# Performance work log

Measured on AMD Instinct MI355X. Metric: run time of the kernel, lower is better.

Reference implementation:

```python
import jax, jax.numpy as jnp
import numpy as np

SOS = 1
V, H, B, T = 32000, 1024, 32, 64


def setup_inputs() -> dict:
    key = jax.random.key(0)
    ks = jax.random.split(key, 9)
    scale = 1.0 / np.sqrt(H)
    return {
        "encoder_outputs": jax.random.normal(ks[0], (B, T, H), dtype=jnp.float32),
        "encoder_hidden": jax.random.normal(ks[1], (1, B, H), dtype=jnp.float32),
        "target_tensor": jax.random.randint(ks[2], (B, T), 0, V),
        "embedding": jax.random.normal(ks[3], (V, H), dtype=jnp.float32),
        "w_ih": jax.random.uniform(ks[4], (3 * H, H), jnp.float32, -scale, scale),
        "w_hh": jax.random.uniform(ks[5], (3 * H, H), jnp.float32, -scale, scale),
        "b_ih": jax.random.uniform(ks[6], (3 * H,), jnp.float32, -scale, scale),
        "b_hh": jax.random.uniform(ks[7], (3 * H,), jnp.float32, -scale, scale),
        "w_out": jax.random.uniform(ks[8], (V, H), jnp.float32, -scale, scale),
        "b_out": jnp.zeros((V,), dtype=jnp.float32),
    }


def _gru_cell(x, h, w_ih, w_hh, b_ih, b_hh):
    # PyTorch GRU cell: gates ordered (r, z, n)
    gi = x @ w_ih.T + b_ih            # [B, 3H]
    gh = h @ w_hh.T + b_hh            # [B, 3H]
    i_r, i_z, i_n = jnp.split(gi, 3, axis=-1)
    h_r, h_z, h_n = jnp.split(gh, 3, axis=-1)
    r = jax.nn.sigmoid(i_r + h_r)
    z = jax.nn.sigmoid(i_z + h_z)
    n = jnp.tanh(i_n + r * h_n)
    return (1.0 - z) * n + z * h


def reference(encoder_outputs, encoder_hidden, target_tensor, embedding,
              w_ih, w_hh, b_ih, b_hh, w_out, b_out):
    batch = encoder_outputs.shape[0]
    # teacher-forced input tokens: [SOS, y_0, ..., y_{T-2}] -> [T, B]
    sos = jnp.full((batch, 1), SOS, dtype=target_tensor.dtype)
    tokens = jnp.concatenate([sos, target_tensor[:, :-1]], axis=1).T  # [T, B]

    h0 = encoder_hidden[0]  # [B, H]

    def step(h, tok):
        x = jax.nn.relu(embedding[tok])            # [B, H]
        h_new = _gru_cell(x, h, w_ih, w_hh, b_ih, b_hh)
        return h_new, h_new

    h_last, hs = jax.lax.scan(step, h0, tokens)    # hs: [T, B, H]
    logits = jnp.einsum('tbh,vh->btv', hs, w_out) + b_out  # [B, T, V]
    log_probs = jax.nn.log_softmax(logits, axis=-1)
    return log_probs, h_last[None]  # hidden returned as [1, B, H]
```

## Files before the change

kernel.cpp:

```cpp
#include <hip/hip_runtime.h>
#include <stdint.h>

#define Hd 1024
#define Bd 32
#define Td 64
#define Vd 32000
#define TB (Td*Bd)
#define G3H 3072
#define NB 64
#define NPOOL 192
#define JC 16
#define NTILE 250
static const size_t BTV = (size_t)Bd * Td * Vd;

typedef unsigned short u16;
typedef __attribute__((ext_vector_type(8))) short bf16x8;
typedef __attribute__((ext_vector_type(4))) float f32x4;
typedef __attribute__((ext_vector_type(4))) unsigned int u32x4;

typedef __attribute__((address_space(3))) void lds_void;
typedef __attribute__((address_space(1))) const void gbl_void;

__device__ __forceinline__ void async_ld16(const void* g, void* l) {
    __builtin_amdgcn_global_load_lds((gbl_void*)g, (lds_void*)l, 16, 0, 0);
}

__device__ __forceinline__ u16 f2bf(float f) {
    union { float f; uint32_t u; } v; v.f = f;
    uint32_t u = v.u;
    return (u16)((u + 0x7fffu + ((u >> 16) & 1u)) >> 16);
}

__device__ __forceinline__ u32x4 gload_b128_sc(const u16* p) {
    u32x4 r;
    asm volatile("global_load_dwordx4 %0, %1, off sc0 sc1"
                 : "=v"(r) : "v"(p) : "memory");
    return r;
}
__device__ __forceinline__ void gstore_b32_sc(u16* p, unsigned int v) {
    asm volatile("global_store_dword %0, %1, off sc0 sc1"
                 :: "v"(p), "v"(v) : "memory");
}
__device__ __forceinline__ void gstore_u32_sc(unsigned int* p, unsigned int v) {
    asm volatile("global_store_dword %0, %1, off sc0 sc1"
                 :: "v"(p), "v"(v) : "memory");
}

__device__ __forceinline__ float fsigmoid(float x) {
    return __builtin_amdgcn_rcpf(1.f + __expf(-x));
}
__device__ __forceinline__ float ftanh(float x) {
    return 1.f - 2.f * __builtin_amdgcn_rcpf(1.f + __expf(2.f * x));
}

__global__ void k_conv_bf16(const float* __restrict__ src, u16* __restrict__ dst, int n4) {
    int i = blockIdx.x * blockDim.x + threadIdx.x;
    if (i >= n4) return;
    float4 f = ((const float4*)src)[i];
    ushort4 o;
    o.x = f2bf(f.x); o.y = f2bf(f.y); o.z = f2bf(f.z); o.w = f2bf(f.w);
    ((ushort4*)dst)[i] = o;
}

__global__ void k_embed(const float* __restrict__ emb, const int* __restrict__ tgt,
                        u16* __restrict__ Xb) {
    int r = blockIdx.x;
    int t = r >> 5, b = r & 31;
    int tok = (t == 0) ? 1 : tgt[b * Td + (t - 1)];
    const float4* srow = (const float4*)(emb + (size_t)tok * Hd);
    int k = threadIdx.x;
    float4 f = srow[k];
    ushort4 o;
    o.x = f2bf(fmaxf(f.x, 0.f)); o.y = f2bf(fmaxf(f.y, 0.f));
    o.z = f2bf(fmaxf(f.z, 0.f)); o.w = f2bf(fmaxf(f.w, 0.f));
    ((ushort4*)(Xb + (size_t)r * Hd))[k] = o;
}

__global__ void k_init_h(const float* __restrict__ eh, u16* __restrict__ hb,
                         unsigned int* __restrict__ cnt) {
    if (blockIdx.x == 0 && threadIdx.x < NB) cnt[threadIdx.x] = 0u;
    int i = blockIdx.x * blockDim.x + threadIdx.x;
    float4 f = ((const float4*)eh)[i];
    ushort4 o;
    o.x = f2bf(f.x); o.y = f2bf(f.y); o.z = f2bf(f.z); o.w = f2bf(f.w);
    ((ushort4*)hb)[i] = o;
}

template<int MODE, int SWAP>
__global__ __launch_bounds__(256, 2)
void k_gemm128(const u16* __restrict__ A, const u16* __restrict__ Bm,
               const float* __restrict__ bias, float* __restrict__ C,
               int N, int K)
{
    __shared__ alignas(16) u16 As[128 * 32];
    __shared__ alignas(16) u16 Bs[128 * 32];
    const int tid  = threadIdx.x;
    const int wave = tid >> 6;
    const int lane = tid & 63;
    const int l16  = lane & 15;
    const int q    = lane >> 4;
    const int wm   = (wave & 1) << 6;
    const int wn   = (wave >> 1) << 6;
    const int tm   = (SWAP ? blockIdx.x : blockIdx.y) << 7;
    const int tn   = (SWAP ? blockIdx.y : blockIdx.x) << 7;

    f32x4 acc[4][4];
#pragma unroll
    for (int i = 0; i < 4; ++i)
#pragma unroll
        for (int j = 0; j < 4; ++j) { f32x4 z = {0.f,0.f,0.f,0.f}; acc[i][j] = z; }

    const int c0 = wave * 2, c1 = wave * 2 + 1;
    const int cr = lane >> 2;
    const int kg = lane & 3;
    const u16* gA0 = A + (size_t)(tm + c0*16 + cr) * K + kg*8;
    const u16* gA1 = A + (size_t)(tm + c1*16 + cr) * K + kg*8;
    const u16* gB0 = Bm + (size_t)(tn + c0*16 + cr) * K + kg*8;
    const u16* gB1 = Bm + (size_t)(tn + c1*16 + cr) * K + kg*8;
    u16* lA0 = &As[c0*512 + lane*8];
    u16* lA1 = &As[c1*512 + lane*8];
    u16* lB0 = &Bs[c0*512 + lane*8];
    u16* lB1 = &Bs[c1*512 + lane*8];

    for (int k0 = 0; k0 < K; k0 += 32) {
        async_ld16(gA0 + k0, lA0);
        async_ld16(gA1 + k0, lA1);
        async_ld16(gB0 + k0, lB0);
        async_ld16(gB1 + k0, lB1);
        __syncthreads();
        bf16x8 af[4], bfr[4];
#pragma unroll
        for (int i = 0; i < 4; ++i)
            af[i] = *(const bf16x8*)&As[(wm + i*16 + l16) * 32 + q*8];
#pragma unroll
        for (int j = 0; j < 4; ++j)
            bfr[j] = *(const bf16x8*)&Bs[(wn + j*16 + l16) * 32 + q*8];
#pragma unroll
        for (int i = 0; i < 4; ++i)
#pragma unroll
            for (int j = 0; j < 4; ++j)
                acc[i][j] = __builtin_amdgcn_mfma_f32_16x16x32_bf16(af[i], bfr[j], acc[i][j], 0, 0, 0);
        __syncthreads();
    }

#pragma unroll
    for (int i = 0; i < 4; ++i) {
        const int mbase = tm + wm + i*16 + q*4;
#pragma unroll
        for (int j = 0; j < 4; ++j) {
            const int n = tn + wn + j*16 + l16;
            const float bv = bias[n];
#pragma unroll
            for (int r = 0; r < 4; ++r) {
                const int m = mbase + r;
                const float v = acc[i][j][r] + bv;
                if (MODE == 0) {
                    C[(size_t)m * N + n] = v;
                } else {
                    const int tt = m >> 5, bb = m & 31;
                    C[(size_t)((bb << 6) + tt) * Vd + n] = v;
                }
            }
        }
    }
}

__global__ __launch_bounds__(256, 1)
void k_gru_logits(const float* __restrict__ gi,
                  const float* __restrict__ enc_h,
                  const u16* __restrict__ w_hhb,
                  const float* __restrict__ b_hh,
                  u16* __restrict__ hbA, u16* __restrict__ hbB,
                  u16* __restrict__ hsb, float* __restrict__ hlast,
                  unsigned int* __restrict__ cnt,
                  const u16* __restrict__ w_outb,
                  const float* __restrict__ b_out,
                  float* __restrict__ out)
{
    __shared__ alignas(16) unsigned char SM[111360];
    const int tid  = threadIdx.x;
    const int wave = tid >> 6, lane = tid & 63;
    const int l16  = lane & 15, q = lane >> 4;

    if (blockIdx.x < NB) {
        u16* Ws = (u16*)SM;
        typedef float ghs_t[3][32][17];
        ghs_t* ghs = (ghs_t*)(SM + 98304);
        const int j0 = blockIdx.x * JC;

        for (int idx = tid; idx < 48 * 128; idx += 256) {
            int gr = idx >> 7;
            int c  = idx & 127;
            const u16* src = w_hhb + (size_t)((gr >> 4) * Hd + j0 + (gr & 15)) * Hd + c * 8;
            *(bf16x8*)&Ws[(size_t)(c * 48 + gr) * 8] = *(const bf16x8*)src;
        }

        const int b  = tid >> 3;
        const int jp = (tid & 7) * 2;
        float h0 = enc_h[b * Hd + j0 + jp];
        float h1 = enc_h[b * Hd + j0 + jp + 1];
        const float br0 = b_hh[j0 + jp],           br1 = b_hh[j0 + jp + 1];
        const float bz0 = b_hh[Hd + j0 + jp],      bz1 = b_hh[Hd + j0 + jp + 1];
        const float bn0 = b_hh[2*Hd + j0 + jp],    bn1 = b_hh[2*Hd + j0 + jp + 1];

        const int mh = wave & 1, kh = wave >> 1;

        float gr0, gr1, gz0, gz1, gn0, gn1;
        {
            const float* gir = gi + (size_t)b * G3H;
            gr0 = gir[j0 + jp];        gr1 = gir[j0 + jp + 1];
            gz0 = gir[Hd + j0 + jp];   gz1 = gir[Hd + j0 + jp + 1];
            gn0 = gir[2*Hd + j0 + jp]; gn1 = gir[2*Hd + j0 + jp + 1];
        }

        __syncthreads();

        for (int t = 0; t < Td; ++t) {
            const u16* hb_in  = (t & 1) ? hbB : hbA;
            u16*       hb_out = (t & 1) ? hbA : hbB;
            const int row = t * 32 + b;

            const u16* ap = hb_in + (size_t)(mh*16 + l16) * Hd + kh*512 + q*8;
            u32x4 areg[16];
#pragma unroll
            for (int it = 0; it < 16; ++it)
                areg[it] = gload_b128_sc(ap + it*32);

            asm volatile("s_waitcnt vmcnt(0)" ::: "memory");

            f32x4 acc0 = {0.f,0.f,0.f,0.f}, acc1 = acc0, acc2 = acc0;
#pragma unroll
            for (int it = 0; it < 16; ++it) {
                bf16x8 a = __builtin_bit_cast(bf16x8, areg[it]);
                const int kgrp = kh*64 + it*4 + q;
                const u16* wp = &Ws[(size_t)(kgrp * 48 + l16) * 8];
                bf16x8 w0 = *(const bf16x8*)(wp);
                bf16x8 w1 = *(const bf16x8*)(wp + 16*8);
                bf16x8 w2 = *(const bf16x8*)(wp + 32*8);
                acc0 = __builtin_amdgcn_mfma_f32_16x16x32_bf16(a, w0, acc0, 0, 0, 0);
                acc1 = __builtin_amdgcn_mfma_f32_16x16x32_bf16(a, w1, acc1, 0, 0, 0);
                acc2 = __builtin_amdgcn_mfma_f32_16x16x32_bf16(a, w2, acc2, 0, 0, 0);
            }
#pragma unroll
            for (int r = 0; r < 4; ++r) {
                const int bb = mh*16 + q*4 + r;
                ghs[kh][0][bb][l16] = acc0[r];
                ghs[kh][1][bb][l16] = acc1[r];
                ghs[kh][2][bb][l16] = acc2[r];
            }
            __syncthreads();

            {
                const float hr0 = ghs[0][0][b][jp]   + ghs[1][0][b][jp]   + br0;
                const float hr1 = ghs[0][0][b][jp+1] + ghs[1][0][b][jp+1] + br1;
                const float hz0 = ghs[0][1][b][jp]   + ghs[1][1][b][jp]   + bz0;
                const float hz1 = ghs[0][1][b][jp+1] + ghs[1][1][b][jp+1] + bz1;
                const float hn0 = ghs[0][2][b][jp]   + ghs[1][2][b][jp]   + bn0;
                const float hn1 = ghs[0][2][b][jp+1] + ghs[1][2][b][jp+1] + bn1;
                const float rg0 = fsigmoid(gr0 + hr0);
                const float rg1 = fsigmoid(gr1 + hr1);
                const float zg0 = fsigmoid(gz0 + hz0);
                const float zg1 = fsigmoid(gz1 + hz1);
                const float ng0 = ftanh(gn0 + rg0 * hn0);
                const float ng1 = ftanh(gn1 + rg1 * hn1);
                h0 = (1.f - zg0) * ng0 + zg0 * h0;
                h1 = (1.f - zg1) * ng1 + zg1 * h1;
                ushort2 pv; pv.x = f2bf(h0); pv.y = f2bf(h1);
                const unsigned int pw = (unsigned int)pv.x | ((unsigned int)pv.y << 16);
                gstore_b32_sc(&hb_out[b * Hd + j0 + jp], pw);
                gstore_b32_sc(&hsb[(size_t)row * Hd + j0 + jp], pw);
                if (t == Td - 1) {
                    hlast[b * Hd + j0 + jp]     = h0;
                    hlast[b * Hd + j0 + jp + 1] = h1;
                }
            }

            __syncthreads();
            if (tid == 0)
                gstore_u32_sc(&cnt[blockIdx.x], (unsigned)(t + 1));

            if (t < Td - 1) {
                {
                    const float* gir = gi + (size_t)((t + 1) * 32 + b) * G3H;
                    gr0 = gir[j0 + jp];        gr1 = gir[j0 + jp + 1];
                    gz0 = gir[Hd + j0 + jp];   gz1 = gir[Hd + j0 + jp + 1];
                    gn0 = gir[2*Hd + j0 + jp]; gn1 = gir[2*Hd + j0 + jp + 1];
                }
                if (wave == 0) {
                    const unsigned tgt = (unsigned)(t + 1);
                    while (!__all(__hip_atomic_load(&cnt[lane], __ATOMIC_RELAXED,
                                                    __HIP_MEMORY_SCOPE_AGENT) >= tgt))
                        __builtin_amdgcn_s_sleep(2);
                }
                __syncthreads();
            }
        }
        return;
    }

    {
        u16* As = (u16*)SM;
        u16* Bs = (u16*)(SM + 32768);
        const int g     = blockIdx.x - NB;
        const int tile0 = g;
        const int tile1 = g + NPOOL;
        const bool two  = (tile1 < NTILE);

        const int wm = (wave & 1) << 6;
        const int wn = (wave >> 1) << 6;
        const int c0 = wave * 2, c1 = wave * 2 + 1;
        const int cr = lane >> 2;
        const int kg = lane & 3;
        const u16* gB0a = w_outb + (size_t)(tile0*128 + c0*16 + cr) * Hd + kg*8;
        const u16* gB1a = w_outb + (size_t)(tile0*128 + c1*16 + cr) * Hd + kg*8;
        const u16* gB0b = w_outb + (size_t)((two ? tile1 : tile0)*128 + c0*16 + cr) * Hd + kg*8;
        const u16* gB1b = w_outb + (size_t)((two ? tile1 : tile0)*128 + c1*16 + cr) * Hd + kg*8;

        const int arow  = tid >> 1;
        const int ahalf = tid & 1;

        for (int G = 0; G < 16; ++G) {
            if (wave == 0) {
                const unsigned tgt = (unsigned)(4 * (G + 1));
                while (!__all(__hip_atomic_load(&cnt[lane], __ATOMIC_RELAXED,
                                                __HIP_MEMORY_SCOPE_AGENT) >= tgt))
                    __builtin_amdgcn_s_sleep(8);
            }
            __syncthreads();

            f32x4 acc0[4][4], acc1[4][4];
#pragma unroll
            for (int i = 0; i < 4; ++i)
#pragma unroll
                for (int j = 0; j < 4; ++j) {
                    f32x4 z = {0.f,0.f,0.f,0.f};
                    acc0[i][j] = z; acc1[i][j] = z;
                }

            const size_t arow0 = (size_t)G * 128;

            for (int s = 0; s < 8; ++s) {
                const int k0 = s * 128;
                const u16* asrc = hsb + (arow0 + arow) * Hd + k0 + ahalf * 64;
                u32x4 ar[8];
#pragma unroll
                for (int j = 0; j < 8; ++j)
                    ar[j] = gload_b128_sc(asrc + j*8);
#pragma unroll
                for (int kc = 0; kc < 4; ++kc) {
                    const int kk = k0 + kc*32;
                    u16* base0 = &Bs[(0*4 + kc) * 4096];
                    async_ld16(gB0a + kk, base0 + c0*512 + lane*8);
                    async_ld16(gB1a + kk, base0 + c1*512 + lane*8);
                    if (two) {
                        u16* base1 = &Bs[(1*4 + kc) * 4096];
                        async_ld16(gB0b + kk, base1 + c0*512 + lane*8);
                        async_ld16(gB1b + kk, base1 + c1*512 + lane*8);
                    }
                }
                asm volatile("s_waitcnt vmcnt(0)" ::: "memory");
#pragma unroll
                for (int j = 0; j < 8; ++j) {
                    const int ob = (ahalf*128 + j*16) ^ ((arow & 7) << 4);
                    *(u32x4*)((unsigned char*)As + arow*256 + ob) = ar[j];
                }
                __syncthreads();

#pragma unroll
                for (int kc = 0; kc < 4; ++kc) {
                    bf16x8 af[4];
#pragma unroll
                    for (int i = 0; i < 4; ++i) {
                        const int row = wm + i*16 + l16;
                        const int ob  = (kc*64 + q*16) ^ ((row & 7) << 4);
                        af[i] = *(const bf16x8*)((const unsigned char*)As + row*256 + ob);
                    }
                    bf16x8 b0[4];
#pragma unroll
                    for (int j = 0; j < 4; ++j)
                        b0[j] = *(const bf16x8*)&Bs[(0*4 + kc)*4096 + (wn + j*16 + l16)*32 + q*8];
#pragma unroll
                    for (int i = 0; i < 4; ++i)
#pragma unroll
                        for (int j = 0; j < 4; ++j)
                            acc0[i][j] = __builtin_amdgcn_mfma_f32_16x16x32_bf16(af[i], b0[j], acc0[i][j], 0, 0, 0);
                    if (two) {
                        bf16x8 b1[4];
#pragma unroll
                        for (int j = 0; j < 4; ++j)
                            b1[j] = *(const bf16x8*)&Bs[(1*4 + kc)*4096 + (wn + j*16 + l16)*32 + q*8];
#pragma unroll
                        for (int i = 0; i < 4; ++i)
#pragma unroll
                            for (int j = 0; j < 4; ++j)
                                acc1[i][j] = __builtin_amdgcn_mfma_f32_16x16x32_bf16(af[i], b1[j], acc1[i][j], 0, 0, 0);
                    }
                }
                __syncthreads();
            }

#pragma unroll
            for (int i = 0; i < 4; ++i) {
                const int lmbase = wm + i*16 + q*4;
#pragma unroll
                for (int j = 0; j < 4; ++j) {
                    const int n0 = tile0*128 + wn + j*16 + l16;
                    const float bv0 = b_out[n0];
#pragma unroll
                    for (int r = 0; r < 4; ++r) {
                        const int gr = (int)(G*128) + lmbase + r;
                        const int tt = gr >> 5, bb = gr & 31;
                        out[(size_t)((bb << 6) + tt) * Vd + n0] = acc0[i][j][r] + bv0;
                    }
                }
            }
            if (two) {
#pragma unroll
                for (int i = 0; i < 4; ++i) {
                    const int lmbase = wm + i*16 + q*4;
#pragma unroll
                    for (int j = 0; j < 4; ++j) {
                        const int n1 = tile1*128 + wn + j*16 + l16;
                        const float bv1 = b_out[n1];
#pragma unroll
                        for (int r = 0; r < 4; ++r) {
                            const int gr = (int)(G*128) + lmbase + r;
                            const int tt = gr >> 5, bb = gr & 31;
                            out[(size_t)((bb << 6) + tt) * Vd + n1] = acc1[i][j][r] + bv1;
                        }
                    }
                }
            }
        }
    }
}

__global__ __launch_bounds__(256)
void k_logsoftmax(float* __restrict__ out) {
    float* row = out + (size_t)blockIdx.x * Vd;
    const int tid = threadIdx.x;
    float m = -1e30f, s = 0.f;
    for (int i = tid * 4; i + 3 < Vd; i += 1024) {
        float4 f = *(const float4*)(row + i);
        float lm = fmaxf(fmaxf(f.x, f.y), fmaxf(f.z, f.w));
        if (lm > m) { s *= __expf(m - lm); m = lm; }
        s += __expf(f.x - m) + __expf(f.y - m) + __expf(f.z - m) + __expf(f.w - m);
    }
    for (int off = 32; off > 0; off >>= 1) {
        float mo = __shfl_down(m, off, 64);
        float so = __shfl_down(s, off, 64);
        float M = fmaxf(m, mo);
        s = s * __expf(m - M) + so * __expf(mo - M);
        m = M;
    }
    __shared__ float sm[4], ss[4];
    const int wave = tid >> 6, lane = tid & 63;
    if (lane == 0) { sm[wave] = m; ss[wave] = s; }
    __syncthreads();
    const float M = fmaxf(fmaxf(sm[0], sm[1]), fmaxf(sm[2], sm[3]));
    const float S = ss[0]*__expf(sm[0]-M) + ss[1]*__expf(sm[1]-M)
                  + ss[2]*__expf(sm[2]-M) + ss[3]*__expf(sm[3]-M);
    const float lz = M + logf(S);
    for (int i = tid * 4; i + 3 < Vd; i += 1024) {
        float4 f = *(const float4*)(row + i);
        f.x -= lz; f.y -= lz; f.z -= lz; f.w -= lz;
        *(float4*)(row + i) = f;
    }
}

extern "C" void kernel_launch(void* const* d_in, const int* in_sizes, int n_in,
                              void* d_out, int out_size, void* d_ws, size_t ws_size,
                              hipStream_t stream) {
    const float* enc_h = (const float*)d_in[1];
    const int*   tgt   = (const int*)d_in[2];
    const float* emb   = (const float*)d_in[3];
    const float* w_ih  = (const float*)d_in[4];
    const float* w_hh  = (const float*)d_in[5];
    const float* b_ih  = (const float*)d_in[6];
    const float* b_hh  = (const float*)d_in[7];
    const float* w_out = (const float*)d_in[8];
    const float* b_out = (const float*)d_in[9];
    float* out = (float*)d_out;

    char* ws = (char*)d_ws;
    size_t off = 0;
    auto alloc = [&](size_t bytes) { void* p = ws + off; off += (bytes + 255) & ~(size_t)255; return p; };
    u16*   w_outb = (u16*)  alloc((size_t)Vd * Hd * 2);
    u16*   w_ihb  = (u16*)  alloc((size_t)G3H * Hd * 2);
    u16*   w_hhb  = (u16*)  alloc((size_t)G3H * Hd * 2);
    u16*   Xb     = (u16*)  alloc((size_t)TB * Hd * 2);
    u16*   hsb    = (u16*)  alloc((size_t)TB * Hd * 2);
    float* gi     = (float*)alloc((size_t)TB * G3H * 4);
    u16*   hb0    = (u16*)  alloc((size_t)Bd * Hd * 2);
    u16*   hb1    = (u16*)  alloc((size_t)Bd * Hd * 2);
    unsigned int* cnt = (unsigned int*) alloc(256);
    (void)ws_size; (void)in_sizes; (void)n_in; (void)out_size;

    k_conv_bf16<<<(Vd*Hd/4 + 255)/256, 256, 0, stream>>>(w_out, w_outb, Vd*Hd/4);
    k_conv_bf16<<<(G3H*Hd/4 + 255)/256, 256, 0, stream>>>(w_ih, w_ihb, G3H*Hd/4);
    k_conv_bf16<<<(G3H*Hd/4 + 255)/256, 256, 0, stream>>>(w_hh, w_hhb, G3H*Hd/4);
    k_embed<<<TB, 256, 0, stream>>>(emb, tgt, Xb);
    k_init_h<<<32, 256, 0, stream>>>(enc_h, hb0, cnt);

    k_gemm128<0,0><<<dim3(G3H/128, TB/128), 256, 0, stream>>>(Xb, w_ihb, b_ih, gi, G3H, Hd);

    k_gru_logits<<<NB + NPOOL, 256, 0, stream>>>(gi, enc_h, w_hhb, b_hh, hb0, hb1,
                                                 hsb, out + BTV, cnt,
                                                 w_outb, b_out, out);

    k_logsoftmax<<<TB, 256, 0, stream>>>(out);
}
```

Before: 1.186 ms.

## Use atomic work queue with double-buffered 256x128 logits tiles in GRU pool

The logits pool blocks now take work items (a 256-row group by 128-column tile) from a global atomic counter, replacing the fixed two-tile assignment per block. Each wave keeps its A fragments in registers and loads them straight from global memory. B tiles are double-buffered in LDS with an XOR swizzle, so the next k-slice can load while MFMAs run. The aim is better load balance across the 250 tiles and overlap of memory with compute. The cost is coarser dependency granularity, since each item waits for 8 GRU steps instead of 4, plus one atomic and two barriers per item.

```diff
diff --git a/kernel.cpp b/kernel.cpp
--- a/kernel.cpp
+++ b/kernel.cpp
@@ -11,6 +11,7 @@
 #define NPOOL 192
 #define JC 16
 #define NTILE 250
+#define NITEMS 2000
 static const size_t BTV = (size_t)Bd * Td * Vd;
 
 typedef unsigned short u16;
@@ -78,7 +79,7 @@
 
 __global__ void k_init_h(const float* __restrict__ eh, u16* __restrict__ hb,
                          unsigned int* __restrict__ cnt) {
-    if (blockIdx.x == 0 && threadIdx.x < NB) cnt[threadIdx.x] = 0u;
+    if (blockIdx.x == 0 && threadIdx.x < 128) cnt[threadIdx.x] = 0u;
     int i = blockIdx.x * blockDim.x + threadIdx.x;
     float4 f = ((const float4*)eh)[i];
     ushort4 o;
@@ -299,135 +300,105 @@
     }
 
     {
-        u16* As = (u16*)SM;
-        u16* Bs = (u16*)(SM + 32768);
-        const int g     = blockIdx.x - NB;
-        const int tile0 = g;
-        const int tile1 = g + NPOOL;
-        const bool two  = (tile1 < NTILE);
-
-        const int wm = (wave & 1) << 6;
-        const int wn = (wave >> 1) << 6;
-        const int c0 = wave * 2, c1 = wave * 2 + 1;
+        u16* Bs = (u16*)SM;
+        volatile unsigned* qw = (volatile unsigned*)(SM + 65536);
         const int cr = lane >> 2;
         const int kg = lane & 3;
-        const u16* gB0a = w_outb + (size_t)(tile0*128 + c0*16 + cr) * Hd + kg*8;
-        const u16* gB1a = w_outb + (size_t)(tile0*128 + c1*16 + cr) * Hd + kg*8;
-        const u16* gB0b = w_outb + (size_t)((two ? tile1 : tile0)*128 + c0*16 + cr) * Hd + kg*8;
-        const u16* gB1b = w_outb + (size_t)((two ? tile1 : tile0)*128 + c1*16 + cr) * Hd + kg*8;
-
-        const int arow  = tid >> 1;
-        const int ahalf = tid & 1;
-
-        for (int G = 0; G < 16; ++G) {
+        const int c0 = wave * 2, c1 = wave * 2 + 1;
+        const int kgs = (kg ^ (cr & 3)) * 8;
+
+        for (;;) {
+            if (tid == 0) *qw = atomicAdd(&cnt[64], 1u);
+            __syncthreads();
+            const unsigned w = *qw;
+            __syncthreads();
+            if (w >= (unsigned)NITEMS) break;
+            const int G8   = (int)(w / (unsigned)NTILE);
+            const int tile = (int)(w % (unsigned)NTILE);
+
             if (wave == 0) {
-                const unsigned tgt = (unsigned)(4 * (G + 1));
+                const unsigned tgt = (unsigned)(8 * (G8 + 1));
                 while (!__all(__hip_atomic_load(&cnt[lane], __ATOMIC_RELAXED,
                                                 __HIP_MEMORY_SCOPE_AGENT) >= tgt))
                     __builtin_amdgcn_s_sleep(8);
             }
             __syncthreads();
 
-            f32x4 acc0[4][4], acc1[4][4];
+            const int rowbase = G8 * 256 + wave * 64;
+            const u16* Ab  = hsb + (size_t)(rowbase + l16) * Hd + q * 8;
+            const u16* Bg0 = w_outb + (size_t)(tile*128 + c0*16 + cr) * Hd + kgs;
+            const u16* Bg1 = w_outb + (size_t)(tile*128 + c1*16 + cr) * Hd + kgs;
+            u16* Bd0 = Bs + (c0*16 + cr)*32 + kg*8;
+            u16* Bd1 = Bs + (c1*16 + cr)*32 + kg*8;
+
+            f32x4 acc[4][8];
 #pragma unroll
             for (int i = 0; i < 4; ++i)
 #pragma unroll
-                for (int j = 0; j < 4; ++j) {
-                    f32x4 z = {0.f,0.f,0.f,0.f};
-                    acc0[i][j] = z; acc1[i][j] = z;
-                }
-
-            const size_t arow0 = (size_t)G * 128;
-
+                for (int j = 0; j < 8; ++j) { f32x4 z = {0.f,0.f,0.f,0.f}; acc[i][j] = z; }
+
+            u32x4 areg[2][4][4];
+#pragma unroll
+            for (int kc = 0; kc < 4; ++kc) {
+                async_ld16(Bg0 + kc*32, Bd0 + kc*4096);
+                async_ld16(Bg1 + kc*32, Bd1 + kc*4096);
+            }
+#pragma unroll
+            for (int i = 0; i < 4; ++i)
+#pragma unroll
+                for (int kc = 0; kc < 4; ++kc)
+                    areg[0][i][kc] = gload_b128_sc(Ab + (size_t)i*16*Hd + kc*32);
+
+#pragma unroll
             for (int s = 0; s < 8; ++s) {
-                const int k0 = s * 128;
-                const u16* asrc = hsb + (arow0 + arow) * Hd + k0 + ahalf * 64;
-                u32x4 ar[8];
-#pragma unroll
-                for (int j = 0; j < 8; ++j)
-                    ar[j] = gload_b128_sc(asrc + j*8);
+                const int cur = s & 1, nxt = cur ^ 1;
+                if (s < 7) {
+                    const int k0 = (s + 1) * 128;
+#pragma unroll
+                    for (int kc = 0; kc < 4; ++kc) {
+                        async_ld16(Bg0 + k0 + kc*32, Bd0 + nxt*16384 + kc*4096);
+                        async_ld16(Bg1 + k0 + kc*32, Bd1 + nxt*16384 + kc*4096);
+                    }
+#pragma unroll
+                    for (int i = 0; i < 4; ++i)
+#pragma unroll
+                        for (int kc = 0; kc < 4; ++kc)
+                            areg[nxt][i][kc] = gload_b128_sc(Ab + (size_t)i*16*Hd + k0 + kc*32);
+                    asm volatile("s_waitcnt vmcnt(24)" ::: "memory");
+                } else {
+                    asm volatile("s_waitcnt vmcnt(0)" ::: "memory");
+                }
+                __builtin_amdgcn_sched_barrier(0);
+                __builtin_amdgcn_s_barrier();
 #pragma unroll
                 for (int kc = 0; kc < 4; ++kc) {
-                    const int kk = k0 + kc*32;
-                    u16* base0 = &Bs[(0*4 + kc) * 4096];
-                    async_ld16(gB0a + kk, base0 + c0*512 + lane*8);
-                    async_ld16(gB1a + kk, base0 + c1*512 + lane*8);
-                    if (two) {
-                        u16* base1 = &Bs[(1*4 + kc) * 4096];
-                        async_ld16(gB0b + kk, base1 + c0*512 + lane*8);
-                        async_ld16(gB1b + kk, base1 + c1*512 + lane*8);
+#pragma unroll
+                    for (int j = 0; j < 8; ++j) {
+                        const int n = j*16 + l16;
+                        const bf16x8 bj = *(const bf16x8*)
+                            &Bs[cur*16384 + kc*4096 + n*32 + (q ^ (n & 3))*8];
+#pragma unroll
+                        for (int i = 0; i < 4; ++i)
+                            acc[i][j] = __builtin_amdgcn_mfma_f32_16x16x32_bf16(
+                                __builtin_bit_cast(bf16x8, areg[cur][i][kc]), bj,
+                                acc[i][j], 0, 0, 0);
                     }
                 }
-                asm volatile("s_waitcnt vmcnt(0)" ::: "memory");
-#pragma unroll
-                for (int j = 0; j < 8; ++j) {
-                    const int ob = (ahalf*128 + j*16) ^ ((arow & 7) << 4);
-                    *(u32x4*)((unsigned char*)As + arow*256 + ob) = ar[j];
-                }
-                __syncthreads();
-
-#pragma unroll
-                for (int kc = 0; kc < 4; ++kc) {
-                    bf16x8 af[4];
-#pragma unroll
-                    for (int i = 0; i < 4; ++i) {
-                        const int row = wm + i*16 + l16;
-                        const int ob  = (kc*64 + q*16) ^ ((row & 7) << 4);
-                        af[i] = *(const bf16x8*)((const unsigned char*)As + row*256 + ob);
-                    }
-                    bf16x8 b0[4];
-#pragma unroll
-                    for (int j = 0; j < 4; ++j)
-                        b0[j] = *(const bf16x8*)&Bs[(0*4 + kc)*4096 + (wn + j*16 + l16)*32 + q*8];
-#pragma unroll
-                    for (int i = 0; i < 4; ++i)
-#pragma unroll
-                        for (int j = 0; j < 4; ++j)
-                            acc0[i][j] = __builtin_amdgcn_mfma_f32_16x16x32_bf16(af[i], b0[j], acc0[i][j], 0, 0, 0);
-                    if (two) {
-                        bf16x8 b1[4];
-#pragma unroll
-                        for (int j = 0; j < 4; ++j)
-                            b1[j] = *(const bf16x8*)&Bs[(1*4 + kc)*4096 + (wn + j*16 + l16)*32 + q*8];
-#pragma unroll
-                        for (int i = 0; i < 4; ++i)
-#pragma unroll
-                            for (int j = 0; j < 4; ++j)
-                                acc1[i][j] = __builtin_amdgcn_mfma_f32_16x16x32_bf16(af[i], b1[j], acc1[i][j], 0, 0, 0);
-                    }
-                }
-                __syncthreads();
-            }
-
-#pragma unroll
-            for (int i = 0; i < 4; ++i) {
-                const int lmbase = wm + i*16 + q*4;
-#pragma unroll
-                for (int j = 0; j < 4; ++j) {
-                    const int n0 = tile0*128 + wn + j*16 + l16;
-                    const float bv0 = b_out[n0];
+                __builtin_amdgcn_s_barrier();
+            }
+
+#pragma unroll
+            for (int j = 0; j < 8; ++j) {
+                const int n = tile*128 + j*16 + l16;
+                const float bv = b_out[n];
+#pragma unroll
+                for (int i = 0; i < 4; ++i) {
+                    const int mbase = rowbase + i*16 + q*4;
 #pragma unroll
                     for (int r = 0; r < 4; ++r) {
-                        const int gr = (int)(G*128) + lmbase + r;
-                        const int tt = gr >> 5, bb = gr & 31;
-                        out[(size_t)((bb << 6) + tt) * Vd + n0] = acc0[i][j][r] + bv0;
-                    }
-                }
-            }
-            if (two) {
-#pragma unroll
-                for (int i = 0; i < 4; ++i) {
-                    const int lmbase = wm + i*16 + q*4;
-#pragma unroll
-                    for (int j = 0; j < 4; ++j) {
-                        const int n1 = tile1*128 + wn + j*16 + l16;
-                        const float bv1 = b_out[n1];
-#pragma unroll
-                        for (int r = 0; r < 4; ++r) {
-                            const int gr = (int)(G*128) + lmbase + r;
-                            const int tt = gr >> 5, bb = gr & 31;
-                            out[(size_t)((bb << 6) + tt) * Vd + n1] = acc1[i][j][r] + bv1;
-                        }
+                        const int m = mbase + r;
+                        const int tt = m >> 5, bb = m & 31;
+                        out[(size_t)((bb << 6) + tt) * Vd + n] = acc[i][j][r] + bv;
                     }
                 }
             }
@@ -493,7 +464,7 @@
     float* gi     = (float*)alloc((size_t)TB * G3H * 4);
     u16*   hb0    = (u16*)  alloc((size_t)Bd * Hd * 2);
     u16*   hb1    = (u16*)  alloc((size_t)Bd * Hd * 2);
-    unsigned int* cnt = (unsigned int*) alloc(256);
+    unsigned int* cnt = (unsigned int*) alloc(512);
     (void)ws_size; (void)in_sizes; (void)n_in; (void)out_size;
 
     k_conv_bf16<<<(Vd*Hd/4 + 255)/256, 256, 0, stream>>>(w_out, w_outb, Vd*Hd/4);
```

Measured after the change: 1.004 ms. -15.3%, faster.
